# Kernel tuning notes

Measured on AMD Instinct MI355X. Metric: run time of the kernel, lower is better.

The kernel has to match this reference:

```python
import jax, jax.numpy as jnp
import numpy as np

B, LIMG, LTXT = 1, 2048, 256
H, NH, HD = 3072, 24, 128
MLP = int(H * 4.0)
EPS = 1e-6


def setup_inputs() -> dict:
    key = jax.random.key(0)
    ks = iter(jax.random.split(key, 64))
    rn = lambda shape, s=0.02: jax.random.normal(next(ks), shape, jnp.float32) * s
    inp = {
        'img': jax.random.normal(next(ks), (B, LIMG, H), jnp.float32),
        'txt': jax.random.normal(next(ks), (B, LTXT, H), jnp.float32),
        'vec': jax.random.normal(next(ks), (B, H), jnp.float32),
        'pe': jax.random.normal(next(ks), (1, 1, LTXT + LIMG, HD // 2, 2, 2), jnp.float32),
    }
    for p in ('img', 'txt'):
        inp[f'{p}_mod_w'] = rn((H, 6 * H)); inp[f'{p}_mod_b'] = jnp.zeros((6 * H,), jnp.float32)
        inp[f'{p}_ln1_s'] = jnp.ones((H,), jnp.float32); inp[f'{p}_ln1_b'] = jnp.zeros((H,), jnp.float32)
        inp[f'{p}_qkv_w'] = rn((H, 3 * H)); inp[f'{p}_qkv_b'] = jnp.zeros((3 * H,), jnp.float32)
        inp[f'{p}_qn'] = jnp.ones((HD,), jnp.float32); inp[f'{p}_kn'] = jnp.ones((HD,), jnp.float32)
        inp[f'{p}_proj_w'] = rn((H, H)); inp[f'{p}_proj_b'] = jnp.zeros((H,), jnp.float32)
        inp[f'{p}_ln2_s'] = jnp.ones((H,), jnp.float32); inp[f'{p}_ln2_b'] = jnp.zeros((H,), jnp.float32)
        inp[f'{p}_mlp_w1'] = rn((H, MLP)); inp[f'{p}_mlp_b1'] = jnp.zeros((MLP,), jnp.float32)
        inp[f'{p}_mlp_w2'] = rn((MLP, H)); inp[f'{p}_mlp_b2'] = jnp.zeros((H,), jnp.float32)
    return inp


def _ln(x, s, b):
    m = jnp.mean(x, -1, keepdims=True)
    v = jnp.mean((x - m) ** 2, -1, keepdims=True)
    return (x - m) * jax.lax.rsqrt(v + EPS) * s + b


def _rms(x, s):
    return x * jax.lax.rsqrt(jnp.mean(x * x, -1, keepdims=True) + EPS) * s


def _apply_rope(x, pe):
    # x: (B,NH,L,HD); pe: (1,1,L,HD/2,2,2)
    xr = x.reshape(*x.shape[:-1], HD // 2, 1, 2)
    out = pe[..., 0] * xr[..., 0] + pe[..., 1] * xr[..., 1]  # (B,NH,L,HD/2,2)
    return out.reshape(x.shape)


def _attention(q, k, v, pe):
    q = _apply_rope(q, pe)
    k = _apply_rope(k, pe)
    scores = jnp.einsum('bhqd,bhkd->bhqk', q, k) / jnp.sqrt(jnp.float32(HD))
    a = jax.nn.softmax(scores, axis=-1)
    x = jnp.einsum('bhqk,bhkd->bhqd', a, v)  # (B,NH,L,HD)
    return x.transpose(0, 2, 1, 3).reshape(x.shape[0], x.shape[2], NH * HD)


def _mod(vec, w, b):
    o = jnp.dot(jax.nn.silu(vec), w) + b          # (B, 6H)
    return jnp.split(o[:, None, :], 6, axis=-1)


def _qkv_heads(x, w, b, qn, kn):
    Bx, L, _ = x.shape
    qkv = (jnp.dot(x, w) + b).reshape(Bx, L, 3, NH, HD).transpose(2, 0, 3, 1, 4)
    q, k, v = qkv[0], qkv[1], qkv[2]
    return _rms(q, qn), _rms(k, kn), v


def reference(img, txt, vec, pe,
              img_mod_w, img_mod_b, img_ln1_s, img_ln1_b, img_qkv_w, img_qkv_b,
              img_qn, img_kn, img_proj_w, img_proj_b, img_ln2_s, img_ln2_b,
              img_mlp_w1, img_mlp_b1, img_mlp_w2, img_mlp_b2,
              txt_mod_w, txt_mod_b, txt_ln1_s, txt_ln1_b, txt_qkv_w, txt_qkv_b,
              txt_qn, txt_kn, txt_proj_w, txt_proj_b, txt_ln2_s, txt_ln2_b,
              txt_mlp_w1, txt_mlp_b1, txt_mlp_w2, txt_mlp_b2):
    i_sh1, i_sc1, i_g1, i_sh2, i_sc2, i_g2 = _mod(vec, img_mod_w, img_mod_b)
    t_sh1, t_sc1, t_g1, t_sh2, t_sc2, t_g2 = _mod(vec, txt_mod_w, txt_mod_b)

    img_mod = (1 + i_sc1) * _ln(img, img_ln1_s, img_ln1_b) + i_sh1
    txt_mod = (1 + t_sc1) * _ln(txt, txt_ln1_s, txt_ln1_b) + t_sh1

    iq, ik, iv = _qkv_heads(img_mod, img_qkv_w, img_qkv_b, img_qn, img_kn)
    tq, tk, tv = _qkv_heads(txt_mod, txt_qkv_w, txt_qkv_b, txt_qn, txt_kn)

    q = jnp.concatenate([tq, iq], axis=2)
    k = jnp.concatenate([tk, ik], axis=2)
    v = jnp.concatenate([tv, iv], axis=2)
    attn = _attention(q, k, v, pe)  # (B, Ltxt+Limg, H)
    Lt = txt.shape[1]
    txt_attn, img_attn = attn[:, :Lt], attn[:, Lt:]

    img = img + i_g1 * (jnp.dot(img_attn, img_proj_w) + img_proj_b)
    h = (1 + i_sc2) * _ln(img, img_ln2_s, img_ln2_b) + i_sh2
    img = img + i_g2 * (jnp.dot(jax.nn.gelu(jnp.dot(h, img_mlp_w1) + img_mlp_b1), img_mlp_w2) + img_mlp_b2)

    txt = txt + t_g1 * (jnp.dot(txt_attn, txt_proj_w) + txt_proj_b)
    h = (1 + t_sc2) * _ln(txt, txt_ln2_s, txt_ln2_b) + t_sh2
    txt = txt + t_g2 * (jnp.dot(jax.nn.gelu(jnp.dot(h, txt_mlp_w1) + txt_mlp_b1), txt_mlp_w2) + txt_mlp_b2)
    return (img, txt)
```

## Files before the change

kernel.cpp:

```cpp
#include <hip/hip_runtime.h>
#include <hip/hip_bf16.h>
#include <cstdint>

typedef __attribute__((ext_vector_type(8))) short s16x8;
typedef __attribute__((ext_vector_type(4))) short s16x4;
typedef __attribute__((ext_vector_type(2))) short s16x2;
typedef __attribute__((ext_vector_type(4))) float f32x4;

#define LTXT 256
#define LIMG 2048
#define LTOT 2304
#define HDIM 3072
#define NHEADS 24
#define HD 128
#define MLPD 12288

__device__ __forceinline__ short f2bf(float f) {
  union { float f; uint32_t u; } v; v.f = f;
  uint32_t r = v.u + 0x7FFFu + ((v.u >> 16) & 1u);
  return (short)(r >> 16);
}
__device__ __forceinline__ float bf2f(short s) {
  union { uint32_t u; float f; } v; v.u = ((uint32_t)(uint16_t)s) << 16;
  return v.f;
}

#define GLDS16(gsrc, ldst)                                                   \
  __builtin_amdgcn_global_load_lds(                                          \
      (const __attribute__((address_space(1))) uint32_t*)(gsrc),             \
      (__attribute__((address_space(3))) uint32_t*)(ldst), 16, 0, 0)

__global__ __launch_bounds__(256)
void wconv(const float* __restrict__ Wf, short* __restrict__ Wt, int K, int N)
{
  __shared__ short Ls[64][68];
  const int t = threadIdx.x;
  const int k0 = blockIdx.x * 64, n0 = blockIdx.y * 64;
  #pragma unroll
  for (int rep = 0; rep < 4; ++rep) {
    int idx = rep * 256 + t;
    int k = idx >> 4;
    int n = (idx & 15) * 4;
    float4 v = *(const float4*)(Wf + (size_t)(k0 + k) * N + n0 + n);
    Ls[k][n + 0] = f2bf(v.x); Ls[k][n + 1] = f2bf(v.y);
    Ls[k][n + 2] = f2bf(v.z); Ls[k][n + 3] = f2bf(v.w);
  }
  __syncthreads();
  #pragma unroll
  for (int rep = 0; rep < 4; ++rep) {
    int idx = rep * 256 + t;
    int n = idx >> 4;
    int k = (idx & 15) * 4;
    s16x4 o = { Ls[k + 0][n], Ls[k + 1][n], Ls[k + 2][n], Ls[k + 3][n] };
    *(s16x4*)(Wt + (size_t)(n0 + n) * K + k0 + k) = o;
  }
}

__global__ __launch_bounds__(256)
void mod_gemv(const float* __restrict__ vec,
              const float* __restrict__ w_img, const float* __restrict__ b_img,
              const float* __restrict__ w_txt, const float* __restrict__ b_txt,
              float* __restrict__ mod_img, float* __restrict__ mod_txt)
{
  __shared__ float sv[HDIM];
  const int t = threadIdx.x;
  for (int i = t; i < HDIM; i += 256) {
    float x = vec[i];
    sv[i] = x / (1.f + __expf(-x));
  }
  __syncthreads();
  const float* w = blockIdx.y ? w_txt : w_img;
  const float* bb = blockIdx.y ? b_txt : b_img;
  float* o = blockIdx.y ? mod_txt : mod_img;
  const int lane = t & 63, kc = t >> 6;
  const int colbase = blockIdx.x * 256 + lane * 4;
  f32x4 acc = {0.f, 0.f, 0.f, 0.f};
  const float* wp = w + (size_t)kc * 768 * 18432 + colbase;
  #pragma unroll 4
  for (int k = 0; k < 768; ++k) {
    float4 wv = *(const float4*)wp;
    float s = sv[kc * 768 + k];
    acc[0] += s * wv.x; acc[1] += s * wv.y;
    acc[2] += s * wv.z; acc[3] += s * wv.w;
    wp += 18432;
  }
  __shared__ f32x4 part[4][64];
  part[kc][lane] = acc;
  __syncthreads();
  if (t < 64) {
    f32x4 r = part[0][t];
    #pragma unroll
    for (int c = 1; c < 4; ++c) r += part[c][t];
    int cb = blockIdx.x * 256 + t * 4;
    float4 bv = *(const float4*)(bb + cb);
    float4 ov; ov.x = r[0] + bv.x; ov.y = r[1] + bv.y;
    ov.z = r[2] + bv.z; ov.w = r[3] + bv.w;
    *(float4*)(o + cb) = ov;
  }
}

__global__ __launch_bounds__(256)
void ln_mod(const float* __restrict__ xi, const float* __restrict__ xt, int rows_img,
            const float* __restrict__ si, const float* __restrict__ bi,
            const float* __restrict__ st, const float* __restrict__ bt,
            const float* __restrict__ modi, const float* __restrict__ modt,
            int sh_chunk, int sc_chunk,
            short* __restrict__ oi, short* __restrict__ ot)
{
  const int row = blockIdx.x;
  const float *x, *s, *b, *mod;
  short* out;
  if (row < rows_img) {
    x = xi + (size_t)row * HDIM; s = si; b = bi; mod = modi;
    out = oi + (size_t)row * HDIM;
  } else {
    int lr = row - rows_img;
    x = xt + (size_t)lr * HDIM; s = st; b = bt; mod = modt;
    out = ot + (size_t)lr * HDIM;
  }
  const float* sh = mod + (size_t)sh_chunk * HDIM;
  const float* sc = mod + (size_t)sc_chunk * HDIM;
  const int t = threadIdx.x;
  float xv[12];
  {
    float4 a = *(const float4*)(x + t * 12 + 0);
    float4 c = *(const float4*)(x + t * 12 + 4);
    float4 d = *(const float4*)(x + t * 12 + 8);
    xv[0]=a.x; xv[1]=a.y; xv[2]=a.z; xv[3]=a.w;
    xv[4]=c.x; xv[5]=c.y; xv[6]=c.z; xv[7]=c.w;
    xv[8]=d.x; xv[9]=d.y; xv[10]=d.z; xv[11]=d.w;
  }
  float sum = 0.f, ss = 0.f;
  #pragma unroll
  for (int e = 0; e < 12; ++e) { sum += xv[e]; ss += xv[e] * xv[e]; }
  for (int xm = 1; xm < 64; xm <<= 1) {
    sum += __shfl_xor(sum, xm);
    ss  += __shfl_xor(ss, xm);
  }
  __shared__ float red[8];
  const int w = t >> 6, lane = t & 63;
  if (lane == 0) { red[w] = sum; red[4 + w] = ss; }
  __syncthreads();
  sum = red[0] + red[1] + red[2] + red[3];
  ss  = red[4] + red[5] + red[6] + red[7];
  const float mean = sum * (1.f / HDIM);
  const float var = ss * (1.f / HDIM) - mean * mean;
  const float rs = rsqrtf(var + 1e-6f);
  short ov[12];
  #pragma unroll
  for (int e = 0; e < 12; ++e) {
    int c = t * 12 + e;
    float y = (xv[e] - mean) * rs * s[c] + b[c];
    ov[e] = f2bf((1.f + sc[c]) * y + sh[c]);
  }
  #pragma unroll
  for (int j = 0; j < 3; ++j) {
    s16x4 v = { ov[j*4+0], ov[j*4+1], ov[j*4+2], ov[j*4+3] };
    *(s16x4*)(out + t * 12 + j * 4) = v;
  }
}

template<int EPI>
__global__ __launch_bounds__(256)
void gemm128(const short* __restrict__ A, int K, int N, int split,
             const short* __restrict__ W0, const short* __restrict__ W1,
             const float* __restrict__ b0, const float* __restrict__ b1,
             void* __restrict__ out0, void* __restrict__ out1,
             const float* __restrict__ r0, const float* __restrict__ r1,
             const float* __restrict__ g0, const float* __restrict__ g1)
{
  __shared__ __align__(16) short lds[16384];
  const int tid = threadIdx.x;
  const int lane = tid & 63, w = tid >> 6;
  const int wr = w >> 1, wc = w & 1;
  const int l15 = lane & 15, lg = lane >> 4;

  const int gx = gridDim.x;
  const int nwg = gx * gridDim.y;
  const int lin = blockIdx.y * gx + blockIdx.x;
  const int q8 = nwg >> 3, r8 = nwg & 7;
  const int xcd = lin & 7, loc = lin >> 3;
  const int nid = (xcd < r8 ? xcd * (q8 + 1) : r8 * (q8 + 1) + (xcd - r8) * q8) + loc;
  const int bm = nid % gx, bn = nid / gx;

  const bool is1 = bm >= split;
  const int m0 = bm * 128, n0 = bn * 128;
  const short* WT = is1 ? W1 : W0;
  const float* bias = is1 ? b1 : b0;
  const int nt = K >> 6;

  f32x4 acc[4][4];
  #pragma unroll
  for (int i = 0; i < 4; ++i)
    #pragma unroll
    for (int j = 0; j < 4; ++j)
      acc[i][j] = f32x4{0.f, 0.f, 0.f, 0.f};

  const int srow_b = w * 8 + (lane >> 3);
  const int x7 = lane & 7;

  for (int t = 0; t < nt; ++t) {
    const size_t kk = (size_t)t * 64;
    __syncthreads();
    #pragma unroll
    for (int rep = 0; rep < 4; ++rep) {
      const int row = rep * 32 + srow_b;
      const int lc = x7 ^ (row & 7);
      GLDS16(A + (size_t)(m0 + row) * K + kk + lc * 8, lds + rep * 2048 + w * 512);
      GLDS16(WT + (size_t)(n0 + row) * K + kk + lc * 8, lds + 8192 + rep * 2048 + w * 512);
    }
    __syncthreads();
    #pragma unroll
    for (int ks = 0; ks < 2; ++ks) {
      const int cofs = ((ks * 4 + lg) ^ (l15 & 7)) * 8;
      s16x8 av[4], bv[4];
      #pragma unroll
      for (int mf = 0; mf < 4; ++mf)
        av[mf] = *(const s16x8*)(lds + (wr * 64 + mf * 16 + l15) * 64 + cofs);
      #pragma unroll
      for (int nf = 0; nf < 4; ++nf)
        bv[nf] = *(const s16x8*)(lds + 8192 + (wc * 64 + nf * 16 + l15) * 64 + cofs);
      #pragma unroll
      for (int mf = 0; mf < 4; ++mf)
        #pragma unroll
        for (int nf = 0; nf < 4; ++nf)
          acc[mf][nf] = __builtin_amdgcn_mfma_f32_16x16x32_bf16(
              av[mf], bv[nf], acc[mf][nf], 0, 0, 0);
    }
  }

  const int lrbase = m0 - (is1 ? split * 128 : 0);
  #pragma unroll
  for (int mf = 0; mf < 4; ++mf)
    #pragma unroll
    for (int nf = 0; nf < 4; ++nf) {
      int col = n0 + wc * 64 + nf * 16 + l15;
      float bvs = bias[col];
      #pragma unroll
      for (int r = 0; r < 4; ++r) {
        int row = lrbase + wr * 64 + mf * 16 + lg * 4 + r;
        float x = acc[mf][nf][r] + bvs;
        if constexpr (EPI == 0) {
          short* o = (short*)(is1 ? out1 : out0);
          o[(size_t)row * N + col] = f2bf(x);
        } else if constexpr (EPI == 1) {
          float g = 0.5f * x * (1.f + tanhf(0.7978845608028654f * (x + 0.044715f * x * x * x)));
          short* o = (short*)(is1 ? out1 : out0);
          o[(size_t)row * N + col] = f2bf(g);
        } else if constexpr (EPI == 2) {
          const float* resid = is1 ? r1 : r0;
          const float* gate = is1 ? g1 : g0;
          float* o = (float*)(is1 ? out1 : out0);
          o[(size_t)row * N + col] = resid[(size_t)row * N + col] + gate[col] * x;
        } else {
          const float* gate = is1 ? g1 : g0;
          float* o = (float*)(is1 ? out1 : out0);
          size_t ix = (size_t)row * N + col;
          o[ix] = o[ix] + gate[col] * x;
        }
      }
    }
}

__global__ __launch_bounds__(256)
void qkvr(const short* __restrict__ qkv, const float* __restrict__ pe,
          const float* __restrict__ qn_img, const float* __restrict__ kn_img,
          const float* __restrict__ qn_txt, const float* __restrict__ kn_txt,
          short* __restrict__ Qh, short* __restrict__ Kh)
{
  const int w = threadIdx.x >> 6, lane = threadIdx.x & 63;
  const int tok = blockIdx.x * 4 + w;
  const int h = blockIdx.y;
  const float* qn = (tok < LTXT) ? qn_txt : qn_img;
  const float* kn = (tok < LTXT) ? kn_txt : kn_img;
  const size_t base = (size_t)tok * 9216 + (size_t)h * HD + lane * 2;
  const float4 p4 = *(const float4*)(pe + ((size_t)tok * 64 + lane) * 4);
  {
    s16x2 qs = *(const s16x2*)(qkv + base);
    float x0 = bf2f(qs[0]), x1 = bf2f(qs[1]);
    float sq = x0 * x0 + x1 * x1;
    for (int xm = 1; xm < 64; xm <<= 1) sq += __shfl_xor(sq, xm);
    float r = rsqrtf(sq * (1.f / HD) + 1e-6f);
    x0 = x0 * r * qn[lane * 2]; x1 = x1 * r * qn[lane * 2 + 1];
    s16x2 o = { f2bf(p4.x * x0 + p4.y * x1), f2bf(p4.z * x0 + p4.w * x1) };
    *(s16x2*)(Qh + ((size_t)h * LTOT + tok) * HD + lane * 2) = o;
  }
  {
    s16x2 ks = *(const s16x2*)(qkv + base + HDIM);
    float x0 = bf2f(ks[0]), x1 = bf2f(ks[1]);
    float sq = x0 * x0 + x1 * x1;
    for (int xm = 1; xm < 64; xm <<= 1) sq += __shfl_xor(sq, xm);
    float r = rsqrtf(sq * (1.f / HD) + 1e-6f);
    x0 = x0 * r * kn[lane * 2]; x1 = x1 * r * kn[lane * 2 + 1];
    s16x2 o = { f2bf(p4.x * x0 + p4.y * x1), f2bf(p4.z * x0 + p4.w * x1) };
    *(s16x2*)(Kh + ((size_t)h * LTOT + tok) * HD + lane * 2) = o;
  }
}

__global__ __launch_bounds__(256)
void vt_k(const short* __restrict__ qkv, short* __restrict__ VT)
{
  __shared__ __align__(16) short Vs[64][136];
  const int h = blockIdx.y, tok0 = blockIdx.x * 64;
  const int t = threadIdx.x;
  #pragma unroll
  for (int rep = 0; rep < 4; ++rep) {
    int idx = rep * 256 + t;
    int tk = idx >> 4, oct = idx & 15;
    *(s16x8*)(&Vs[tk][oct * 8]) =
        *(const s16x8*)(qkv + (size_t)(tok0 + tk) * 9216 + 6144 + (size_t)h * HD + oct * 8);
  }
  __syncthreads();
  #pragma unroll
  for (int rep = 0; rep < 4; ++rep) {
    int idx = rep * 256 + t;
    int d = idx >> 3, tg = idx & 7;
    s16x8 o;
    #pragma unroll
    for (int j = 0; j < 8; ++j) o[j] = Vs[tg * 8 + j][d];
    *(s16x8*)(VT + ((size_t)h * HD + d) * LTOT + tok0 + tg * 8) = o;
  }
}

__global__ __launch_bounds__(256, 2)
void attn_k(const short* __restrict__ Qh, const short* __restrict__ Kh,
            const short* __restrict__ VT, short* __restrict__ out)
{
  __shared__ __align__(16) short Ps[4][32][72];
  const int t = threadIdx.x, lane = t & 63, w = t >> 6;
  const int l15 = lane & 15, lg = lane >> 4;
  const int h = blockIdx.y;
  const int qrow = blockIdx.x * 128 + w * 32;

  s16x8 qf[2][4];
  #pragma unroll
  for (int mf = 0; mf < 2; ++mf)
    #pragma unroll
    for (int ks = 0; ks < 4; ++ks)
      qf[mf][ks] = *(const s16x8*)(Qh + ((size_t)h * LTOT + qrow + mf * 16 + l15) * HD + ks * 32 + lg * 8);

  f32x4 O[2][8];
  #pragma unroll
  for (int mf = 0; mf < 2; ++mf)
    #pragma unroll
    for (int dt = 0; dt < 8; ++dt) O[mf][dt] = f32x4{0.f, 0.f, 0.f, 0.f};
  float mrow[2][4], lrow[2][4];
  #pragma unroll
  for (int mf = 0; mf < 2; ++mf)
    #pragma unroll
    for (int r = 0; r < 4; ++r) { mrow[mf][r] = -1e30f; lrow[mf][r] = 0.f; }

  for (int kt = 0; kt < LTOT / 64; ++kt) {
    const int k0 = kt * 64;
    f32x4 S[2][4];
    #pragma unroll
    for (int mf = 0; mf < 2; ++mf)
      #pragma unroll
      for (int jt = 0; jt < 4; ++jt) S[mf][jt] = f32x4{0.f, 0.f, 0.f, 0.f};
    #pragma unroll
    for (int ks = 0; ks < 4; ++ks)
      #pragma unroll
      for (int jt = 0; jt < 4; ++jt) {
        s16x8 kf = *(const s16x8*)(Kh + ((size_t)h * LTOT + k0 + jt * 16 + l15) * HD + ks * 32 + lg * 8);
        S[0][jt] = __builtin_amdgcn_mfma_f32_16x16x32_bf16(qf[0][ks], kf, S[0][jt], 0, 0, 0);
        S[1][jt] = __builtin_amdgcn_mfma_f32_16x16x32_bf16(qf[1][ks], kf, S[1][jt], 0, 0, 0);
      }
    #pragma unroll
    for (int mf = 0; mf < 2; ++mf) {
      const float scl = 0.08838834764831845f;
      #pragma unroll
      for (int jt = 0; jt < 4; ++jt) S[mf][jt] *= scl;
      float pm[4];
      #pragma unroll
      for (int r = 0; r < 4; ++r)
        pm[r] = fmaxf(fmaxf(S[mf][0][r], S[mf][1][r]), fmaxf(S[mf][2][r], S[mf][3][r]));
      for (int xm = 1; xm < 16; xm <<= 1)
        #pragma unroll
        for (int r = 0; r < 4; ++r) pm[r] = fmaxf(pm[r], __shfl_xor(pm[r], xm));
      f32x4 corrv;
      #pragma unroll
      for (int r = 0; r < 4; ++r) {
        float mn = fmaxf(mrow[mf][r], pm[r]);
        corrv[r] = __expf(mrow[mf][r] - mn);
        mrow[mf][r] = mn;
      }
      float rs[4] = {0.f, 0.f, 0.f, 0.f};
      #pragma unroll
      for (int jt = 0; jt < 4; ++jt)
        #pragma unroll
        for (int r = 0; r < 4; ++r) {
          float p = __expf(S[mf][jt][r] - mrow[mf][r]);
          S[mf][jt][r] = p;
          rs[r] += p;
        }
      for (int xm = 1; xm < 16; xm <<= 1)
        #pragma unroll
        for (int r = 0; r < 4; ++r) rs[r] += __shfl_xor(rs[r], xm);
      #pragma unroll
      for (int r = 0; r < 4; ++r) lrow[mf][r] = lrow[mf][r] * corrv[r] + rs[r];
      #pragma unroll
      for (int dt = 0; dt < 8; ++dt) O[mf][dt] *= corrv;
      #pragma unroll
      for (int jt = 0; jt < 4; ++jt)
        #pragma unroll
        for (int r = 0; r < 4; ++r)
          Ps[w][mf * 16 + lg * 4 + r][jt * 16 + l15] = f2bf(S[mf][jt][r]);
    }
    asm volatile("s_waitcnt lgkmcnt(0)" ::: "memory");
    __builtin_amdgcn_sched_barrier(0);
    #pragma unroll
    for (int kk2 = 0; kk2 < 2; ++kk2) {
      s16x8 pf0 = *(const s16x8*)(&Ps[w][l15][kk2 * 32 + lg * 8]);
      s16x8 pf1 = *(const s16x8*)(&Ps[w][16 + l15][kk2 * 32 + lg * 8]);
      #pragma unroll
      for (int dt = 0; dt < 8; ++dt) {
        s16x8 vf = *(const s16x8*)(VT + ((size_t)h * HD + dt * 16 + l15) * LTOT + k0 + kk2 * 32 + lg * 8);
        O[0][dt] = __builtin_amdgcn_mfma_f32_16x16x32_bf16(pf0, vf, O[0][dt], 0, 0, 0);
        O[1][dt] = __builtin_amdgcn_mfma_f32_16x16x32_bf16(pf1, vf, O[1][dt], 0, 0, 0);
      }
    }
    asm volatile("s_waitcnt lgkmcnt(0)" ::: "memory");
    __builtin_amdgcn_sched_barrier(0);
  }
  #pragma unroll
  for (int mf = 0; mf < 2; ++mf) {
    f32x4 inv;
    #pragma unroll
    for (int r = 0; r < 4; ++r) inv[r] = 1.f / lrow[mf][r];
    #pragma unroll
    for (int dt = 0; dt < 8; ++dt) {
      f32x4 o = O[mf][dt] * inv;
      #pragma unroll
      for (int r = 0; r < 4; ++r)
        out[(size_t)(qrow + mf * 16 + lg * 4 + r) * HDIM + (size_t)h * HD + dt * 16 + l15] = f2bf(o[r]);
    }
  }
}

extern "C" void kernel_launch(void* const* d_in, const int* in_sizes, int n_in,
                              void* d_out, int out_size, void* d_ws, size_t ws_size,
                              hipStream_t stream)
{
  (void)in_sizes; (void)n_in; (void)out_size;
  const float* img = (const float*)d_in[0];
  const float* txt = (const float*)d_in[1];
  const float* vec = (const float*)d_in[2];
  const float* pe  = (const float*)d_in[3];
  const float* Pi[16]; const float* Pt[16];
  for (int i = 0; i < 16; ++i) Pi[i] = (const float*)d_in[4 + i];
  for (int i = 0; i < 16; ++i) Pt[i] = (const float*)d_in[20 + i];

  char* ws = (char*)d_ws;
  float* MODI = (float*)(ws + 0);
  float* MODT = (float*)(ws + 73728);
  short* XMI  = (short*)(ws + 147456);
  short* XMT  = (short*)(ws + 12730368);
  short* QKV  = (short*)(ws + 14303232);
  short* QHh  = (short*)(ws + 56770560);
  short* KHh  = (short*)(ws + 70926336);
  short* VTt  = (short*)(ws + 85082112);
  short* ATT  = (short*)(ws + 99237888);
  short* H1   = (short*)(ws + 14303232);
  short* WTA  = (short*)(ws + 113393664);
  short* WTB  = (short*)(ws + 188891136);
  if (ws_size < (size_t)264388608) return;
  float* outI = (float*)d_out;
  float* outT = outI + (size_t)LIMG * HDIM;

  mod_gemv<<<dim3(72, 2), 256, 0, stream>>>(vec, Pi[0], Pi[1], Pt[0], Pt[1], MODI, MODT);
  ln_mod<<<dim3(LTOT), 256, 0, stream>>>(img, txt, LIMG, Pi[2], Pi[3], Pt[2], Pt[3],
                                         MODI, MODT, 0, 1, XMI, XMT);
  wconv<<<dim3(48, 144), 256, 0, stream>>>(Pi[4], WTA, HDIM, 3 * HDIM);
  wconv<<<dim3(48, 144), 256, 0, stream>>>(Pt[4], WTB, HDIM, 3 * HDIM);
  gemm128<0><<<dim3(18, 72), 256, 0, stream>>>(XMI, HDIM, 3 * HDIM, 16,
      WTA, WTB, Pi[5], Pt[5],
      QKV + (size_t)LTXT * 9216, QKV, nullptr, nullptr, nullptr, nullptr);
  qkvr<<<dim3(LTOT / 4, NHEADS), 256, 0, stream>>>(QKV, pe, Pi[6], Pi[7], Pt[6], Pt[7], QHh, KHh);
  vt_k<<<dim3(LTOT / 64, NHEADS), 256, 0, stream>>>(QKV, VTt);
  attn_k<<<dim3(LTOT / 128, NHEADS), 256, 0, stream>>>(QHh, KHh, VTt, ATT);
  wconv<<<dim3(48, 48), 256, 0, stream>>>(Pt[8], WTA, HDIM, HDIM);
  wconv<<<dim3(48, 48), 256, 0, stream>>>(Pi[8], WTB, HDIM, HDIM);
  gemm128<2><<<dim3(18, 24), 256, 0, stream>>>(ATT, HDIM, HDIM, 2,
      WTA, WTB, Pt[9], Pi[9], outT, outI, txt, img,
      MODT + 2 * HDIM, MODI + 2 * HDIM);
  ln_mod<<<dim3(LTOT), 256, 0, stream>>>(outI, outT, LIMG, Pi[10], Pi[11], Pt[10], Pt[11],
                                         MODI, MODT, 3, 4, XMI, XMT);
  wconv<<<dim3(48, 192), 256, 0, stream>>>(Pi[12], WTA, HDIM, MLPD);
  wconv<<<dim3(48, 192), 256, 0, stream>>>(Pt[12], WTB, HDIM, MLPD);
  gemm128<1><<<dim3(18, 96), 256, 0, stream>>>(XMI, HDIM, MLPD, 16,
      WTA, WTB, Pi[13], Pt[13],
      H1, H1 + (size_t)LIMG * MLPD, nullptr, nullptr, nullptr, nullptr);
  wconv<<<dim3(192, 48), 256, 0, stream>>>(Pi[14], WTA, MLPD, HDIM);
  wconv<<<dim3(192, 48), 256, 0, stream>>>(Pt[14], WTB, MLPD, HDIM);
  gemm128<3><<<dim3(18, 24), 256, 0, stream>>>(H1, MLPD, HDIM, 16,
      WTA, WTB, Pi[15], Pt[15], outI, outT, nullptr, nullptr,
      MODI + 5 * HDIM, MODT + 5 * HDIM);
}
```

Before: 1.537 ms.

## Fuse fp32 weight conversion and transpose into GEMM B-tile loading

Removes the separate wconv kernels that converted fp32 weights to transposed bf16 in workspace, and has the GEMM load fp32 weight tiles directly, converting to bf16 and transposing into swizzled LDS. This drops one write and one read of every weight matrix plus eight kernel launches. In exchange, each M-tile block rereads fp32 weights (twice the bytes of bf16) many times and the B load becomes synchronous register-staged stores rather than async global_load_lds, which may stall the MFMA loop.

```diff
diff --git a/kernel.cpp b/kernel.cpp
--- a/kernel.cpp
+++ b/kernel.cpp
@@ -20,6 +20,10 @@
   uint32_t r = v.u + 0x7FFFu + ((v.u >> 16) & 1u);
   return (short)(r >> 16);
 }
+__device__ __forceinline__ short bfc(float f) {
+  __hip_bfloat16 h = __float2bfloat16(f);
+  return *reinterpret_cast<short*>(&h);
+}
 __device__ __forceinline__ float bf2f(short s) {
   union { uint32_t u; float f; } v; v.u = ((uint32_t)(uint16_t)s) << 16;
   return v.f;
@@ -29,32 +33,6 @@
   __builtin_amdgcn_global_load_lds(                                          \
       (const __attribute__((address_space(1))) uint32_t*)(gsrc),             \
       (__attribute__((address_space(3))) uint32_t*)(ldst), 16, 0, 0)
-
-__global__ __launch_bounds__(256)
-void wconv(const float* __restrict__ Wf, short* __restrict__ Wt, int K, int N)
-{
-  __shared__ short Ls[64][68];
-  const int t = threadIdx.x;
-  const int k0 = blockIdx.x * 64, n0 = blockIdx.y * 64;
-  #pragma unroll
-  for (int rep = 0; rep < 4; ++rep) {
-    int idx = rep * 256 + t;
-    int k = idx >> 4;
-    int n = (idx & 15) * 4;
-    float4 v = *(const float4*)(Wf + (size_t)(k0 + k) * N + n0 + n);
-    Ls[k][n + 0] = f2bf(v.x); Ls[k][n + 1] = f2bf(v.y);
-    Ls[k][n + 2] = f2bf(v.z); Ls[k][n + 3] = f2bf(v.w);
-  }
-  __syncthreads();
-  #pragma unroll
-  for (int rep = 0; rep < 4; ++rep) {
-    int idx = rep * 256 + t;
-    int n = idx >> 4;
-    int k = (idx & 15) * 4;
-    s16x4 o = { Ls[k + 0][n], Ls[k + 1][n], Ls[k + 2][n], Ls[k + 3][n] };
-    *(s16x4*)(Wt + (size_t)(n0 + n) * K + k0 + k) = o;
-  }
-}
 
 __global__ __launch_bounds__(256)
 void mod_gemv(const float* __restrict__ vec,
@@ -162,14 +140,15 @@
 
 template<int EPI>
 __global__ __launch_bounds__(256)
-void gemm128(const short* __restrict__ A, int K, int N, int split,
-             const short* __restrict__ W0, const short* __restrict__ W1,
-             const float* __restrict__ b0, const float* __restrict__ b1,
-             void* __restrict__ out0, void* __restrict__ out1,
-             const float* __restrict__ r0, const float* __restrict__ r1,
-             const float* __restrict__ g0, const float* __restrict__ g1)
-{
-  __shared__ __align__(16) short lds[16384];
+void gemmF(const short* __restrict__ A, int K, int N, int split,
+           const float* __restrict__ W0, const float* __restrict__ W1,
+           const float* __restrict__ b0, const float* __restrict__ b1,
+           void* __restrict__ out0, void* __restrict__ out1,
+           const float* __restrict__ r0, const float* __restrict__ r1,
+           const float* __restrict__ g0, const float* __restrict__ g1)
+{
+  __shared__ __align__(16) short ldsA[8192];
+  __shared__ __align__(16) short ldsB[8192];
   const int tid = threadIdx.x;
   const int lane = tid & 63, w = tid >> 6;
   const int wr = w >> 1, wc = w & 1;
@@ -185,7 +164,7 @@
 
   const bool is1 = bm >= split;
   const int m0 = bm * 128, n0 = bn * 128;
-  const short* WT = is1 ? W1 : W0;
+  const float* Wf = is1 ? W1 : W0;
   const float* bias = is1 ? b1 : b0;
   const int nt = K >> 6;
 
@@ -198,6 +177,8 @@
 
   const int srow_b = w * 8 + (lane >> 3);
   const int x7 = lane & 7;
+  const int nq = tid & 31;
+  const int kq_b = tid >> 5;
 
   for (int t = 0; t < nt; ++t) {
     const size_t kk = (size_t)t * 64;
@@ -206,8 +187,21 @@
     for (int rep = 0; rep < 4; ++rep) {
       const int row = rep * 32 + srow_b;
       const int lc = x7 ^ (row & 7);
-      GLDS16(A + (size_t)(m0 + row) * K + kk + lc * 8, lds + rep * 2048 + w * 512);
-      GLDS16(WT + (size_t)(n0 + row) * K + kk + lc * 8, lds + 8192 + rep * 2048 + w * 512);
+      GLDS16(A + (size_t)(m0 + row) * K + kk + lc * 8, ldsA + rep * 2048 + w * 512);
+    }
+    #pragma unroll
+    for (int pass = 0; pass < 2; ++pass) {
+      const int kq = pass * 8 + kq_b;
+      f32x4 wv[4];
+      #pragma unroll
+      for (int i = 0; i < 4; ++i)
+        wv[i] = *(const f32x4*)(Wf + (size_t)(kk + kq * 4 + i) * N + n0 + nq * 4);
+      #pragma unroll
+      for (int j = 0; j < 4; ++j) {
+        const int n = nq * 4 + j;
+        s16x4 o = { bfc(wv[0][j]), bfc(wv[1][j]), bfc(wv[2][j]), bfc(wv[3][j]) };
+        *(s16x4*)(ldsB + n * 64 + (((kq >> 1) ^ (n & 7)) * 8 + (kq & 1) * 4)) = o;
+      }
     }
     __syncthreads();
     #pragma unroll
@@ -216,10 +210,10 @@
       s16x8 av[4], bv[4];
       #pragma unroll
       for (int mf = 0; mf < 4; ++mf)
-        av[mf] = *(const s16x8*)(lds + (wr * 64 + mf * 16 + l15) * 64 + cofs);
+        av[mf] = *(const s16x8*)(ldsA + (wr * 64 + mf * 16 + l15) * 64 + cofs);
       #pragma unroll
       for (int nf = 0; nf < 4; ++nf)
-        bv[nf] = *(const s16x8*)(lds + 8192 + (wc * 64 + nf * 16 + l15) * 64 + cofs);
+        bv[nf] = *(const s16x8*)(ldsB + (wc * 64 + nf * 16 + l15) * 64 + cofs);
       #pragma unroll
       for (int mf = 0; mf < 4; ++mf)
         #pragma unroll
@@ -461,38 +455,28 @@
   short* VTt  = (short*)(ws + 85082112);
   short* ATT  = (short*)(ws + 99237888);
   short* H1   = (short*)(ws + 14303232);
-  short* WTA  = (short*)(ws + 113393664);
-  short* WTB  = (short*)(ws + 188891136);
-  if (ws_size < (size_t)264388608) return;
+  if (ws_size < (size_t)113393664) return;
   float* outI = (float*)d_out;
   float* outT = outI + (size_t)LIMG * HDIM;
 
   mod_gemv<<<dim3(72, 2), 256, 0, stream>>>(vec, Pi[0], Pi[1], Pt[0], Pt[1], MODI, MODT);
   ln_mod<<<dim3(LTOT), 256, 0, stream>>>(img, txt, LIMG, Pi[2], Pi[3], Pt[2], Pt[3],
                                          MODI, MODT, 0, 1, XMI, XMT);
-  wconv<<<dim3(48, 144), 256, 0, stream>>>(Pi[4], WTA, HDIM, 3 * HDIM);
-  wconv<<<dim3(48, 144), 256, 0, stream>>>(Pt[4], WTB, HDIM, 3 * HDIM);
-  gemm128<0><<<dim3(18, 72), 256, 0, stream>>>(XMI, HDIM, 3 * HDIM, 16,
-      WTA, WTB, Pi[5], Pt[5],
+  gemmF<0><<<dim3(18, 72), 256, 0, stream>>>(XMI, HDIM, 3 * HDIM, 16,
+      Pi[4], Pt[4], Pi[5], Pt[5],
       QKV + (size_t)LTXT * 9216, QKV, nullptr, nullptr, nullptr, nullptr);
   qkvr<<<dim3(LTOT / 4, NHEADS), 256, 0, stream>>>(QKV, pe, Pi[6], Pi[7], Pt[6], Pt[7], QHh, KHh);
   vt_k<<<dim3(LTOT / 64, NHEADS), 256, 0, stream>>>(QKV, VTt);
   attn_k<<<dim3(LTOT / 128, NHEADS), 256, 0, stream>>>(QHh, KHh, VTt, ATT);
-  wconv<<<dim3(48, 48), 256, 0, stream>>>(Pt[8], WTA, HDIM, HDIM);
-  wconv<<<dim3(48, 48), 256, 0, stream>>>(Pi[8], WTB, HDIM, HDIM);
-  gemm128<2><<<dim3(18, 24), 256, 0, stream>>>(ATT, HDIM, HDIM, 2,
-      WTA, WTB, Pt[9], Pi[9], outT, outI, txt, img,
+  gemmF<2><<<dim3(18, 24), 256, 0, stream>>>(ATT, HDIM, HDIM, 2,
+      Pt[8], Pi[8], Pt[9], Pi[9], outT, outI, txt, img,
       MODT + 2 * HDIM, MODI + 2 * HDIM);
   ln_mod<<<dim3(LTOT), 256, 0, stream>>>(outI, outT, LIMG, Pi[10], Pi[11], Pt[10], Pt[11],
                                          MODI, MODT, 3, 4, XMI, XMT);
-  wconv<<<dim3(48, 192), 256, 0, stream>>>(Pi[12], WTA, HDIM, MLPD);
-  wconv<<<dim3(48, 192), 256, 0, stream>>>(Pt[12], WTB, HDIM, MLPD);
-  gemm128<1><<<dim3(18, 96), 256, 0, stream>>>(XMI, HDIM, MLPD, 16,
-      WTA, WTB, Pi[13], Pt[13],
+  gemmF<1><<<dim3(18, 96), 256, 0, stream>>>(XMI, HDIM, MLPD, 16,
+      Pi[12], Pt[12], Pi[13], Pt[13],
       H1, H1 + (size_t)LIMG * MLPD, nullptr, nullptr, nullptr, nullptr);
-  wconv<<<dim3(192, 48), 256, 0, stream>>>(Pi[14], WTA, MLPD, HDIM);
-  wconv<<<dim3(192, 48), 256, 0, stream>>>(Pt[14], WTB, MLPD, HDIM);
-  gemm128<3><<<dim3(18, 24), 256, 0, stream>>>(H1, MLPD, HDIM, 16,
-      WTA, WTB, Pi[15], Pt[15], outI, outT, nullptr, nullptr,
+  gemmF<3><<<dim3(18, 24), 256, 0, stream>>>(H1, MLPD, HDIM, 16,
+      Pi[14], Pt[14], Pi[15], Pt[15], outI, outT, nullptr, nullptr,
       MODI + 5 * HDIM, MODT + 5 * HDIM);
 }
```

Result: slower. 1.829 ms (+19.0%).
